# Performance work log

Measured on AMD Instinct MI355X. Metric: run time of the kernel, lower is better.

Reference implementation:

```python
import jax, jax.numpy as jnp
import numpy as np

N_EMBD = 768
N_HEAD = 12
HEAD_DIM = N_EMBD // N_HEAD
EPS = 1e-6


def setup_inputs() -> dict:
    key = jax.random.key(0)
    ks = jax.random.split(key, 8)
    B, T, C = 4, 2048, N_EMBD
    s = 0.02
    return {
        "x": jax.random.normal(ks[0], (B, T, C), jnp.float32),
        "ln1_w": jnp.ones((C,), jnp.float32),
        "ln1_b": jnp.zeros((C,), jnp.float32),
        "W_attn": jax.random.normal(ks[1], (C, 3 * C), jnp.float32) * s,
        "b_attn": jnp.zeros((3 * C,), jnp.float32),
        "W_attn_proj": jax.random.normal(ks[2], (C, C), jnp.float32) * s,
        "b_attn_proj": jnp.zeros((C,), jnp.float32),
        "ln2_w": jnp.ones((C,), jnp.float32),
        "ln2_b": jnp.zeros((C,), jnp.float32),
        "W_fc": jax.random.normal(ks[3], (C, 4 * C), jnp.float32) * s,
        "b_fc": jnp.zeros((4 * C,), jnp.float32),
        "W_mlp_proj": jax.random.normal(ks[4], (4 * C, C), jnp.float32) * s,
        "b_mlp_proj": jnp.zeros((C,), jnp.float32),
    }


def layer_norm(x, w, b):
    # Faithful to MyLayerNorm: (x - mean) / (std + eps), std with ddof=0
    mean = jnp.mean(x, axis=-1, keepdims=True)
    std = jnp.sqrt(jnp.mean((x - mean) ** 2, axis=-1, keepdims=True))
    return w * (x - mean) / (std + EPS) + b


def attention(h, W_attn, b_attn, W_proj, b_proj):
    B, T, C = h.shape
    qkv = h @ W_attn + b_attn                      # [B,T,3C]
    q, k, v = jnp.split(qkv, 3, axis=-1)
    # [B,T,C] -> [B,H,T,D]
    def to_heads(t):
        return t.reshape(B, T, N_HEAD, HEAD_DIM).transpose(0, 2, 1, 3)
    q, k, v = to_heads(q), to_heads(k), to_heads(v)
    att = jnp.einsum("bhtd,bhsd->bhts", q, k) * (1.0 / np.sqrt(HEAD_DIM))
    causal = jnp.tril(jnp.ones((T, T), bool))[None, None]
    att = jnp.where(causal, att, -jnp.inf)
    att = jax.nn.softmax(att, axis=-1)
    y = jnp.einsum("bhts,bhsd->bhtd", att, v)      # [B,H,T,D]
    y = y.transpose(0, 2, 1, 3).reshape(B, T, C)
    return y @ W_proj + b_proj


def mlp(h, W_fc, b_fc, W_proj, b_proj):
    h = jax.nn.gelu(h @ W_fc + b_fc, approximate=False)
    return h @ W_proj + b_proj


def reference(x, ln1_w, ln1_b, W_attn, b_attn, W_attn_proj, b_attn_proj,
              ln2_w, ln2_b, W_fc, b_fc, W_mlp_proj, b_mlp_proj):
    x = x + attention(layer_norm(x, ln1_w, ln1_b), W_attn, b_attn, W_attn_proj, b_attn_proj)
    x = x + mlp(layer_norm(x, ln2_w, ln2_b), W_fc, b_fc, W_mlp_proj, b_mlp_proj)
    return x
```

## Files before the change

### kernel.cpp

```cpp
#include <hip/hip_runtime.h>
#include <hip/hip_bf16.h>
#include <math.h>

#define N_EMBD 768
#define N_HEAD 12
#define HEAD_DIM 64
#define TOKENS 8192
#define SEQ 2048
#define BATCH 4
#define NQT (SEQ / 64)

typedef __attribute__((ext_vector_type(8))) short short8;
typedef __attribute__((ext_vector_type(4))) short short4v;
typedef __attribute__((ext_vector_type(4))) float f32x4;

__device__ __forceinline__ short f2bf(float f) {
    unsigned u = __builtin_bit_cast(unsigned, f);
    unsigned r = (u + 0x7fffu + ((u >> 16) & 1u)) >> 16;
    return (short)r;
}
__device__ __forceinline__ short f2bf_fast(float f) {
    unsigned u = __builtin_bit_cast(unsigned, f);
    return (short)((u + 0x8000u) >> 16);
}

__device__ __forceinline__ float gelu_fast(float x) {
    float z = 1.5957691216057308f * x * (1.0f + 0.044715f * x * x);
    return x / (1.0f + __expf(-z));
}

__device__ __forceinline__ void gld16(const void* g, void* l) {
    __builtin_amdgcn_global_load_lds(
        (const __attribute__((address_space(1))) unsigned int*)g,
        (__attribute__((address_space(3))) unsigned int*)l, 16, 0, 0);
}

__global__ __launch_bounds__(256) void wT_all(
        const float* __restrict__ Wa, short* __restrict__ Ta,
        const float* __restrict__ Wp, short* __restrict__ Tp,
        const float* __restrict__ Wf, short* __restrict__ Tf,
        const float* __restrict__ Wm, short* __restrict__ Tm) {
    __shared__ float T[32][33];
    int id = blockIdx.x;
    const float* W; short* Wt; int K, N;
    if (id < 1728)      { W = Wa; Wt = Ta; K = 768;  N = 2304; }
    else if (id < 2304) { W = Wp; Wt = Tp; K = 768;  N = 768;  id -= 1728; }
    else if (id < 4608) { W = Wf; Wt = Tf; K = 768;  N = 3072; id -= 2304; }
    else                { W = Wm; Wt = Tm; K = 3072; N = 768;  id -= 4608; }
    int tn = N >> 5;
    int n0 = (id % tn) * 32, k0 = (id / tn) * 32;
    int c = threadIdx.x & 31, r0 = threadIdx.x >> 5;
#pragma unroll
    for (int i = 0; i < 32; i += 8)
        T[r0 + i][c] = W[(size_t)(k0 + r0 + i) * N + n0 + c];
    __syncthreads();
#pragma unroll
    for (int i = 0; i < 32; i += 8)
        Wt[(size_t)(n0 + r0 + i) * K + k0 + c] = f2bf(T[c][r0 + i]);
}

__global__ __launch_bounds__(256) void ln_bf_kernel(const float* __restrict__ x,
                                                    const float* __restrict__ w,
                                                    const float* __restrict__ b,
                                                    short* __restrict__ out) {
    int row = blockIdx.x * 4 + (threadIdx.x >> 6);
    int lane = threadIdx.x & 63;
    const float4* xr = (const float4*)(x + (size_t)row * N_EMBD);
    const float4* wr = (const float4*)w;
    const float4* br = (const float4*)b;

    float4 v[3];
#pragma unroll
    for (int i = 0; i < 3; ++i) v[i] = xr[lane + 64 * i];
    float s = 0.f;
#pragma unroll
    for (int i = 0; i < 3; ++i) s += v[i].x + v[i].y + v[i].z + v[i].w;
#pragma unroll
    for (int off = 1; off < 64; off <<= 1) s += __shfl_xor(s, off, 64);
    float mean = s * (1.f / 768.f);

    float var = 0.f;
#pragma unroll
    for (int i = 0; i < 3; ++i) {
        float a0 = v[i].x - mean, a1 = v[i].y - mean,
              a2 = v[i].z - mean, a3 = v[i].w - mean;
        var += a0 * a0 + a1 * a1 + a2 * a2 + a3 * a3;
    }
#pragma unroll
    for (int off = 1; off < 64; off <<= 1) var += __shfl_xor(var, off, 64);
    float inv = 1.f / (sqrtf(var * (1.f / 768.f)) + 1e-6f);

    short4v* yr = (short4v*)(out + (size_t)row * N_EMBD);
#pragma unroll
    for (int i = 0; i < 3; ++i) {
        float4 wv = wr[lane + 64 * i], bv = br[lane + 64 * i];
        short4v o;
        o[0] = f2bf(wv.x * (v[i].x - mean) * inv + bv.x);
        o[1] = f2bf(wv.y * (v[i].y - mean) * inv + bv.y);
        o[2] = f2bf(wv.z * (v[i].z - mean) * inv + bv.z);
        o[3] = f2bf(wv.w * (v[i].w - mean) * inv + bv.w);
        yr[lane + 64 * i] = o;
    }
}

template <int ACT, int VOUT, int SWAP>
__global__ __launch_bounds__(256) void gemm_mfma(
        const short* __restrict__ A,
        const short* __restrict__ Bt,
        const float* __restrict__ bias,
        short* __restrict__ outp,
        short* __restrict__ vt,
        int M, int N, int K) {
    __shared__ short As[8192];
    __shared__ short Bs[8192];
    int tid = threadIdx.x;
    int wave = tid >> 6, lane = tid & 63;
    int quad = lane >> 4, l15 = lane & 15;
    int m0 = blockIdx.x * 128, n0 = blockIdx.y * 128;
    int wm = wave >> 1, wn = wave & 1;
    int sr = lane >> 2, sc = (lane & 3) * 8;

    f32x4 acc[4][4];
#pragma unroll
    for (int i = 0; i < 4; ++i)
#pragma unroll
        for (int j = 0; j < 4; ++j) acc[i][j] = (f32x4){0.f, 0.f, 0.f, 0.f};

    const short* ag = A + (size_t)(m0 + wave * 32 + sr) * K + sc;
    const short* bg = Bt + (size_t)(n0 + wave * 32 + sr) * K + sc;
    int woff = wave * 1024;
    int nk = K >> 5;

    auto stage = [&](int t) {
        int nb = (t & 1) * 4096 + woff;
        int kn = t << 5;
        gld16(ag + kn, &As[nb]);
        gld16(ag + kn + (size_t)16 * K, &As[nb + 512]);
        gld16(bg + kn, &Bs[nb]);
        gld16(bg + kn + (size_t)16 * K, &Bs[nb + 512]);
    };

    stage(0);
    if (nk > 1) stage(1);

    for (int it = 0; it < nk; ++it) {
        if (it + 1 < nk) asm volatile("s_waitcnt vmcnt(4)" ::: "memory");
        else             asm volatile("s_waitcnt vmcnt(0)" ::: "memory");
        __builtin_amdgcn_s_barrier();
        __builtin_amdgcn_sched_barrier(0);
        int cb = (it & 1) * 4096;
        short8 af[4], bfr[4];
#pragma unroll
        for (int mt = 0; mt < 4; ++mt)
            af[mt] = *(const short8*)&As[cb + (wm * 64 + mt * 16 + l15) * 32 + quad * 8];
#pragma unroll
        for (int nt = 0; nt < 4; ++nt)
            bfr[nt] = *(const short8*)&Bs[cb + (wn * 64 + nt * 16 + l15) * 32 + quad * 8];
        asm volatile("s_waitcnt lgkmcnt(0)" ::: "memory");
        __builtin_amdgcn_sched_barrier(0);
        __builtin_amdgcn_s_setprio(1);
#pragma unroll
        for (int mt = 0; mt < 4; ++mt)
#pragma unroll
            for (int nt = 0; nt < 4; ++nt) {
                if (SWAP)
                    acc[mt][nt] = __builtin_amdgcn_mfma_f32_16x16x32_bf16(
                        bfr[nt], af[mt], acc[mt][nt], 0, 0, 0);
                else
                    acc[mt][nt] = __builtin_amdgcn_mfma_f32_16x16x32_bf16(
                        af[mt], bfr[nt], acc[mt][nt], 0, 0, 0);
            }
        __builtin_amdgcn_s_setprio(0);
        __builtin_amdgcn_sched_barrier(0);
        __builtin_amdgcn_s_barrier();
        if (it + 2 < nk) stage(it + 2);
    }

    if (SWAP) {
#pragma unroll
        for (int nt = 0; nt < 4; ++nt) {
            int colb = n0 + wn * 64 + nt * 16 + quad * 4;
            f32x4 b4 = *(const f32x4*)&bias[colb];
#pragma unroll
            for (int mt = 0; mt < 4; ++mt) {
                int row = m0 + wm * 64 + mt * 16 + l15;
                short4v o4;
#pragma unroll
                for (int r = 0; r < 4; ++r) {
                    float v = acc[mt][nt][r] + b4[r];
                    if (ACT) v = gelu_fast(v);
                    o4[r] = f2bf(v);
                }
                *(short4v*)&outp[(size_t)row * N + colb] = o4;
            }
        }
        return;
    }

    if (VOUT && n0 >= 1536) {
#pragma unroll
        for (int mt = 0; mt < 4; ++mt) {
            int row0 = m0 + wm * 64 + mt * 16 + quad * 4;
            int b = row0 >> 11, t0 = row0 & 2047;
#pragma unroll
            for (int nt = 0; nt < 4; ++nt) {
                int col = n0 + wn * 64 + nt * 16 + l15;
                int vcol = col - 1536;
                int bh = b * N_HEAD + (vcol >> 6);
                int d = vcol & 63;
                float bi = bias[col];
                short4v o;
#pragma unroll
                for (int r = 0; r < 4; ++r) o[r] = f2bf(acc[mt][nt][r] + bi);
                *(short4v*)&vt[((size_t)bh * 64 + d) * SEQ + t0] = o;
            }
        }
        return;
    }

#pragma unroll
    for (int mt = 0; mt < 4; ++mt) {
        int row0 = m0 + wm * 64 + mt * 16 + quad * 4;
#pragma unroll
        for (int nt = 0; nt < 4; ++nt) {
            int col = n0 + wn * 64 + nt * 16 + l15;
            float bi = bias[col];
#pragma unroll
            for (int r = 0; r < 4; ++r) {
                float v = acc[mt][nt][r] + bi;
                if (ACT) v = gelu_fast(v);
                outp[(size_t)(row0 + r) * N + col] = f2bf(v);
            }
        }
    }
}

__global__ __launch_bounds__(256) void gemm_mfma_n64(
        const short* __restrict__ A,
        const short* __restrict__ Bt,
        const float* __restrict__ bias,
        const float* __restrict__ res,
        float* __restrict__ outp,
        int M, int N, int K) {
    __shared__ short As[8192];
    __shared__ short Bs[4096];
    int tid = threadIdx.x;
    int wave = tid >> 6, lane = tid & 63;
    int quad = lane >> 4, l15 = lane & 15;
    int m0 = blockIdx.x * 128, n0 = blockIdx.y * 64;
    int wm = wave >> 1, wn = wave & 1;
    int sr = lane >> 2, sc = (lane & 3) * 8;

    f32x4 acc[4][2];
#pragma unroll
    for (int i = 0; i < 4; ++i)
#pragma unroll
        for (int j = 0; j < 2; ++j) acc[i][j] = (f32x4){0.f, 0.f, 0.f, 0.f};

    const short* gptr[3];
    int loff[3];
    bool isa[3];
#pragma unroll
    for (int j = 0; j < 3; ++j) {
        int c = wave * 3 + j;
        if (c < 8) {
            gptr[j] = A + (size_t)(m0 + c * 16 + sr) * K + sc;
            loff[j] = c * 512; isa[j] = true;
        } else {
            gptr[j] = Bt + (size_t)(n0 + (c - 8) * 16 + sr) * K + sc;
            loff[j] = (c - 8) * 512; isa[j] = false;
        }
    }
    int nk = K >> 5;

    auto stage = [&](int t) {
        int nba = (t & 1) * 4096, nbb = (t & 1) * 2048;
        int kn = t << 5;
#pragma unroll
        for (int j = 0; j < 3; ++j)
            gld16(gptr[j] + kn, isa[j] ? &As[nba + loff[j]] : &Bs[nbb + loff[j]]);
    };

    stage(0);
    if (nk > 1) stage(1);

    for (int it = 0; it < nk; ++it) {
        if (it + 1 < nk) asm volatile("s_waitcnt vmcnt(3)" ::: "memory");
        else             asm volatile("s_waitcnt vmcnt(0)" ::: "memory");
        __builtin_amdgcn_s_barrier();
        __builtin_amdgcn_sched_barrier(0);
        int cba = (it & 1) * 4096, cbb = (it & 1) * 2048;
        short8 af[4], bfr[2];
#pragma unroll
        for (int mt = 0; mt < 4; ++mt)
            af[mt] = *(const short8*)&As[cba + (wm * 64 + mt * 16 + l15) * 32 + quad * 8];
#pragma unroll
        for (int nt = 0; nt < 2; ++nt)
            bfr[nt] = *(const short8*)&Bs[cbb + (wn * 32 + nt * 16 + l15) * 32 + quad * 8];
        asm volatile("s_waitcnt lgkmcnt(0)" ::: "memory");
        __builtin_amdgcn_sched_barrier(0);
        __builtin_amdgcn_s_setprio(1);
#pragma unroll
        for (int mt = 0; mt < 4; ++mt)
#pragma unroll
            for (int nt = 0; nt < 2; ++nt)
                acc[mt][nt] = __builtin_amdgcn_mfma_f32_16x16x32_bf16(
                    bfr[nt], af[mt], acc[mt][nt], 0, 0, 0);
        __builtin_amdgcn_s_setprio(0);
        __builtin_amdgcn_sched_barrier(0);
        __builtin_amdgcn_s_barrier();
        if (it + 2 < nk) stage(it + 2);
    }

#pragma unroll
    for (int nt = 0; nt < 2; ++nt) {
        int colb = n0 + wn * 32 + nt * 16 + quad * 4;
        f32x4 b4 = *(const f32x4*)&bias[colb];
#pragma unroll
        for (int mt = 0; mt < 4; ++mt) {
            int row = m0 + wm * 64 + mt * 16 + l15;
            f32x4 rv = *(const f32x4*)&res[(size_t)row * N + colb];
            f32x4 ov;
#pragma unroll
            for (int r = 0; r < 4; ++r) ov[r] = acc[mt][nt][r] + b4[r] + rv[r];
            *(f32x4*)&outp[(size_t)row * N + colb] = ov;
        }
    }
}

template <bool DIAG>
__device__ __forceinline__ void attn_kt(
        const short* __restrict__ Ks, const short* __restrict__ Vs,
        short* __restrict__ Ps, int cb,
        const short8* qf, short8 ones,
        f32x4* o, f32x4& lacc,
        int wave, int quad, int l15, int pswz) {
    f32x4 sacc[4];
#pragma unroll
    for (int nt = 0; nt < 4; ++nt) sacc[nt] = (f32x4){0.f, 0.f, 0.f, 0.f};
#pragma unroll
    for (int nt = 0; nt < 4; ++nt)
#pragma unroll
        for (int ks = 0; ks < 2; ++ks) {
            short8 kf = *(const short8*)&Ks[cb + ks * 2048 + (nt * 16 + l15) * 32 + quad * 8];
            sacc[nt] = __builtin_amdgcn_mfma_f32_16x16x32_bf16(qf[ks], kf, sacc[nt], 0, 0, 0);
        }

#pragma unroll
    for (int nt = 0; nt < 4; ++nt) {
        int scol = nt * 16 + l15;
        int base = (scol >> 5) * 2048 + (scol & 31);
#pragma unroll
        for (int r = 0; r < 4; ++r) {
            float p = exp2f(fmaf(sacc[nt][r], 0.18033688011112042f,
                                 -5.770780163555854f));
            if (DIAG && (scol > wave * 16 + quad * 4 + r)) p = 0.f;
            Ps[(base + (wave * 16 + quad * 4 + r) * 32) ^ (quad << 4)] = f2bf_fast(p);
        }
    }

    short8 pf0 = *(const short8*)&Ps[((wave * 16 + l15) * 32 + quad * 8) ^ pswz];
    short8 pf1 = *(const short8*)&Ps[(2048 + (wave * 16 + l15) * 32 + quad * 8) ^ pswz];
    lacc = __builtin_amdgcn_mfma_f32_16x16x32_bf16(pf0, ones, lacc, 0, 0, 0);
    lacc = __builtin_amdgcn_mfma_f32_16x16x32_bf16(pf1, ones, lacc, 0, 0, 0);
#pragma unroll
    for (int nt = 0; nt < 4; ++nt) {
        short8 vf0 = *(const short8*)&Vs[cb + (nt * 16 + l15) * 32 + quad * 8];
        short8 vf1 = *(const short8*)&Vs[cb + 2048 + (nt * 16 + l15) * 32 + quad * 8];
        o[nt] = __builtin_amdgcn_mfma_f32_16x16x32_bf16(pf0, vf0, o[nt], 0, 0, 0);
        o[nt] = __builtin_amdgcn_mfma_f32_16x16x32_bf16(pf1, vf1, o[nt], 0, 0, 0);
    }
}

__device__ __forceinline__ void attn_tile(
        const short* __restrict__ qkv, const short* __restrict__ Vt,
        short* __restrict__ y, int bh, int qt,
        short* Ks, short* Vs, short* Ps) {
    int tid = threadIdx.x;
    int wave = tid >> 6, lane = tid & 63;
    int quad = lane >> 4, l15 = lane & 15;
    int h = bh % N_HEAD, b = bh / N_HEAD;
    size_t bT = (size_t)b * SEQ;
    int q0 = qt * 64;
    int sr = lane >> 2, sc = (lane & 3) * 8;

    const short ONE_BF = (short)0x3F80;
    short8 ones;
#pragma unroll
    for (int j = 0; j < 8; ++j) ones[j] = ONE_BF;

    const short* qrow = qkv + (bT + q0 + wave * 16 + l15) * 2304 + h * 64 + quad * 8;
    short8 qf[2];
    qf[0] = *(const short8*)qrow;
    qf[1] = *(const short8*)(qrow + 32);

    __syncthreads();
#pragma unroll
    for (int j = 0; j < 4; ++j) {
        int c = wave * 4 + j;
        if (c < 8) {
            int sub = c >> 2, r0 = (c & 3) * 16;
            const short* g = qkv + (bT + r0 + sr) * 2304 + 768 + h * 64 + sub * 32 + sc;
            gld16(g, &Ks[sub * 2048 + r0 * 32]);
        } else {
            int cv = c - 8;
            int sub = cv >> 2, r0 = (cv & 3) * 16;
            const short* g = Vt + ((size_t)bh * 64 + r0 + sr) * SEQ + sub * 32 + sc;
            gld16(g, &Vs[sub * 2048 + r0 * 32]);
        }
    }
    __syncthreads();

    f32x4 o[4];
#pragma unroll
    for (int nt = 0; nt < 4; ++nt) o[nt] = (f32x4){0.f, 0.f, 0.f, 0.f};
    f32x4 lacc = (f32x4){0.f, 0.f, 0.f, 0.f};

    const int pswz = ((l15 >> 2) & 3) << 4;

    for (int kt = 0; kt < qt; ++kt) {
        int cb = (kt & 1) * 4096;
        if (kt) __syncthreads();
        int nb = ((kt + 1) & 1) * 4096;
        int k0n = (kt + 1) * 64;
#pragma unroll
        for (int j = 0; j < 4; ++j) {
            int c = wave * 4 + j;
            if (c < 8) {
                int sub = c >> 2, r0 = (c & 3) * 16;
                const short* g = qkv + (bT + k0n + r0 + sr) * 2304 + 768 + h * 64 + sub * 32 + sc;
                gld16(g, &Ks[nb + sub * 2048 + r0 * 32]);
            } else {
                int cv = c - 8;
                int sub = cv >> 2, r0 = (cv & 3) * 16;
                const short* g = Vt + ((size_t)bh * 64 + r0 + sr) * SEQ + k0n + sub * 32 + sc;
                gld16(g, &Vs[nb + sub * 2048 + r0 * 32]);
            }
        }
        attn_kt<false>(Ks, Vs, Ps, cb, qf, ones, o, lacc, wave, quad, l15, pswz);
    }

    if (qt) __syncthreads();
    attn_kt<true>(Ks, Vs, Ps, (qt & 1) * 4096, qf, ones, o, lacc,
                  wave, quad, l15, pswz);

    float inv[4];
#pragma unroll
    for (int r = 0; r < 4; ++r) inv[r] = 1.f / lacc[r];
#pragma unroll
    for (int nt = 0; nt < 4; ++nt)
#pragma unroll
        for (int r = 0; r < 4; ++r)
            y[(bT + q0 + wave * 16 + quad * 4 + r) * N_EMBD + h * 64 + nt * 16 + l15] =
                f2bf(o[nt][r] * inv[r]);
}

__global__ __launch_bounds__(256, 4) void attn_mfma(
        const short* __restrict__ qkv, const short* __restrict__ Vt,
        short* __restrict__ y) {
    __shared__ short Ks[8192], Vs[8192], Ps[4096];
    int bh = blockIdx.x;
    int pair = blockIdx.y;
    attn_tile(qkv, Vt, y, bh, pair, Ks, Vs, Ps);
    attn_tile(qkv, Vt, y, bh, NQT - 1 - pair, Ks, Vs, Ps);
}

extern "C" void kernel_launch(void* const* d_in, const int* in_sizes, int n_in,
                              void* d_out, int out_size, void* d_ws, size_t ws_size,
                              hipStream_t stream) {
    const float* x         = (const float*)d_in[0];
    const float* ln1_w     = (const float*)d_in[1];
    const float* ln1_b     = (const float*)d_in[2];
    const float* W_attn    = (const float*)d_in[3];
    const float* b_attn    = (const float*)d_in[4];
    const float* W_attn_pr = (const float*)d_in[5];
    const float* b_attn_pr = (const float*)d_in[6];
    const float* ln2_w     = (const float*)d_in[7];
    const float* ln2_b     = (const float*)d_in[8];
    const float* W_fc      = (const float*)d_in[9];
    const float* b_fc      = (const float*)d_in[10];
    const float* W_mlp_pr  = (const float*)d_in[11];
    const float* b_mlp_pr  = (const float*)d_in[12];
    float* out = (float*)d_out;

    const int M = TOKENS, C = N_EMBD;
    char* ws = (char*)d_ws;
    size_t region0 = (size_t)M * 3072 * 2;
    short* qkv_bf = (short*)ws;
    short* fc_bf  = (short*)ws;
    size_t off = region0;
    short* VtB   = (short*)(ws + off); off += (size_t)48 * 64 * SEQ * 2;
    short* yb    = (short*)(ws + off); off += (size_t)M * C * 2;
    short* lnb   = (short*)(ws + off); off += (size_t)M * C * 2;
    float* x1    = (float*)(ws + off); off += (size_t)M * C * 4;
    short* WaT   = (short*)(ws + off); off += (size_t)2304 * 768 * 2;
    short* WpT   = (short*)(ws + off); off += (size_t)768 * 768 * 2;
    short* WfT   = (short*)(ws + off); off += (size_t)3072 * 768 * 2;
    short* WmT   = (short*)(ws + off); off += (size_t)768 * 3072 * 2;

    wT_all<<<6912, 256, 0, stream>>>(W_attn, WaT, W_attn_pr, WpT,
                                     W_fc, WfT, W_mlp_pr, WmT);

    ln_bf_kernel<<<M / 4, 256, 0, stream>>>(x, ln1_w, ln1_b, lnb);

    gemm_mfma<0, 1, 0><<<dim3(M / 128, 2304 / 128), 256, 0, stream>>>(
        lnb, WaT, b_attn, qkv_bf, VtB, M, 2304, 768);

    attn_mfma<<<dim3(BATCH * N_HEAD, NQT / 2), 256, 0, stream>>>(qkv_bf, VtB, yb);

    gemm_mfma_n64<<<dim3(M / 128, 768 / 64), 256, 0, stream>>>(
        yb, WpT, b_attn_pr, x, x1, M, 768, 768);

    ln_bf_kernel<<<M / 4, 256, 0, stream>>>(x1, ln2_w, ln2_b, lnb);

    gemm_mfma<1, 0, 1><<<dim3(M / 128, 3072 / 128), 256, 0, stream>>>(
        lnb, WfT, b_fc, fc_bf, nullptr, M, 3072, 768);

    gemm_mfma_n64<<<dim3(M / 128, 768 / 64), 256, 0, stream>>>(
        fc_bf, WmT, b_mlp_pr, x1, out, M, 768, 3072);
}
```

Baseline: 389.7 us.

## Switch GEMM main loops to single-barrier double buffering and deepen n64 K-step

```diff
diff --git a/kernel.cpp b/kernel.cpp
--- a/kernel.cpp
+++ b/kernel.cpp
@@ -129,26 +129,24 @@
     const short* ag = A + (size_t)(m0 + wave * 32 + sr) * K + sc;
     const short* bg = Bt + (size_t)(n0 + wave * 32 + sr) * K + sc;
     int woff = wave * 1024;
+
+    gld16(ag, &As[woff]);
+    gld16(ag + (size_t)16 * K, &As[woff + 512]);
+    gld16(bg, &Bs[woff]);
+    gld16(bg + (size_t)16 * K, &Bs[woff + 512]);
+
     int nk = K >> 5;
-
-    auto stage = [&](int t) {
-        int nb = (t & 1) * 4096 + woff;
-        int kn = t << 5;
-        gld16(ag + kn, &As[nb]);
-        gld16(ag + kn + (size_t)16 * K, &As[nb + 512]);
-        gld16(bg + kn, &Bs[nb]);
-        gld16(bg + kn + (size_t)16 * K, &Bs[nb + 512]);
-    };
-
-    stage(0);
-    if (nk > 1) stage(1);
-
     for (int it = 0; it < nk; ++it) {
-        if (it + 1 < nk) asm volatile("s_waitcnt vmcnt(4)" ::: "memory");
-        else             asm volatile("s_waitcnt vmcnt(0)" ::: "memory");
-        __builtin_amdgcn_s_barrier();
-        __builtin_amdgcn_sched_barrier(0);
         int cb = (it & 1) * 4096;
+        __syncthreads();
+        if (it + 1 < nk) {
+            int nb = ((it + 1) & 1) * 4096 + woff;
+            int kn = (it + 1) << 5;
+            gld16(ag + kn, &As[nb]);
+            gld16(ag + kn + (size_t)16 * K, &As[nb + 512]);
+            gld16(bg + kn, &Bs[nb]);
+            gld16(bg + kn + (size_t)16 * K, &Bs[nb + 512]);
+        }
         short8 af[4], bfr[4];
 #pragma unroll
         for (int mt = 0; mt < 4; ++mt)
@@ -156,9 +154,6 @@
 #pragma unroll
         for (int nt = 0; nt < 4; ++nt)
             bfr[nt] = *(const short8*)&Bs[cb + (wn * 64 + nt * 16 + l15) * 32 + quad * 8];
-        asm volatile("s_waitcnt lgkmcnt(0)" ::: "memory");
-        __builtin_amdgcn_sched_barrier(0);
-        __builtin_amdgcn_s_setprio(1);
 #pragma unroll
         for (int mt = 0; mt < 4; ++mt)
 #pragma unroll
@@ -170,10 +165,6 @@
                     acc[mt][nt] = __builtin_amdgcn_mfma_f32_16x16x32_bf16(
                         af[mt], bfr[nt], acc[mt][nt], 0, 0, 0);
             }
-        __builtin_amdgcn_s_setprio(0);
-        __builtin_amdgcn_sched_barrier(0);
-        __builtin_amdgcn_s_barrier();
-        if (it + 2 < nk) stage(it + 2);
     }
 
     if (SWAP) {
@@ -242,8 +233,8 @@
         const float* __restrict__ res,
         float* __restrict__ outp,
         int M, int N, int K) {
-    __shared__ short As[8192];
-    __shared__ short Bs[4096];
+    __shared__ short As[16384];
+    __shared__ short Bs[8192];
     int tid = threadIdx.x;
     int wave = tid >> 6, lane = tid & 63;
     int quad = lane >> 4, l15 = lane & 15;
@@ -257,59 +248,57 @@
 #pragma unroll
         for (int j = 0; j < 2; ++j) acc[i][j] = (f32x4){0.f, 0.f, 0.f, 0.f};
 
-    const short* gptr[3];
-    int loff[3];
-    bool isa[3];
-#pragma unroll
-    for (int j = 0; j < 3; ++j) {
-        int c = wave * 3 + j;
-        if (c < 8) {
-            gptr[j] = A + (size_t)(m0 + c * 16 + sr) * K + sc;
-            loff[j] = c * 512; isa[j] = true;
+    const short* gptr[6];
+    int loff[6];
+    bool isa[6];
+#pragma unroll
+    for (int j = 0; j < 6; ++j) {
+        int c = wave * 6 + j;
+        if (c < 16) {
+            int ks = c >> 3, r0 = (c & 7) * 16;
+            gptr[j] = A + (size_t)(m0 + r0 + sr) * K + ks * 32 + sc;
+            loff[j] = ks * 4096 + r0 * 32; isa[j] = true;
         } else {
-            gptr[j] = Bt + (size_t)(n0 + (c - 8) * 16 + sr) * K + sc;
-            loff[j] = (c - 8) * 512; isa[j] = false;
-        }
-    }
-    int nk = K >> 5;
+            int cb = c - 16;
+            int ks = cb >> 2, r0 = (cb & 3) * 16;
+            gptr[j] = Bt + (size_t)(n0 + r0 + sr) * K + ks * 32 + sc;
+            loff[j] = ks * 2048 + r0 * 32; isa[j] = false;
+        }
+    }
+    int nk = K >> 6;
 
     auto stage = [&](int t) {
-        int nba = (t & 1) * 4096, nbb = (t & 1) * 2048;
-        int kn = t << 5;
-#pragma unroll
-        for (int j = 0; j < 3; ++j)
-            gld16(gptr[j] + kn, isa[j] ? &As[nba + loff[j]] : &Bs[nbb + loff[j]]);
+        int ba = (t & 1) << 13, bb = (t & 1) << 12;
+        int kn = t << 6;
+#pragma unroll
+        for (int j = 0; j < 6; ++j)
+            gld16(gptr[j] + kn, isa[j] ? &As[ba + loff[j]] : &Bs[bb + loff[j]]);
     };
 
     stage(0);
-    if (nk > 1) stage(1);
 
     for (int it = 0; it < nk; ++it) {
-        if (it + 1 < nk) asm volatile("s_waitcnt vmcnt(3)" ::: "memory");
-        else             asm volatile("s_waitcnt vmcnt(0)" ::: "memory");
-        __builtin_amdgcn_s_barrier();
-        __builtin_amdgcn_sched_barrier(0);
-        int cba = (it & 1) * 4096, cbb = (it & 1) * 2048;
-        short8 af[4], bfr[2];
-#pragma unroll
-        for (int mt = 0; mt < 4; ++mt)
-            af[mt] = *(const short8*)&As[cba + (wm * 64 + mt * 16 + l15) * 32 + quad * 8];
-#pragma unroll
-        for (int nt = 0; nt < 2; ++nt)
-            bfr[nt] = *(const short8*)&Bs[cbb + (wn * 32 + nt * 16 + l15) * 32 + quad * 8];
-        asm volatile("s_waitcnt lgkmcnt(0)" ::: "memory");
-        __builtin_amdgcn_sched_barrier(0);
-        __builtin_amdgcn_s_setprio(1);
-#pragma unroll
-        for (int mt = 0; mt < 4; ++mt)
+        int cba = (it & 1) << 13, cbb = (it & 1) << 12;
+        __syncthreads();
+        if (it + 1 < nk) stage(it + 1);
+#pragma unroll
+        for (int ks = 0; ks < 2; ++ks) {
+            short8 af[4], bfr[2];
+#pragma unroll
+            for (int mt = 0; mt < 4; ++mt)
+                af[mt] = *(const short8*)&As[cba + ks * 4096 +
+                                             (wm * 64 + mt * 16 + l15) * 32 + quad * 8];
 #pragma unroll
             for (int nt = 0; nt < 2; ++nt)
-                acc[mt][nt] = __builtin_amdgcn_mfma_f32_16x16x32_bf16(
-                    bfr[nt], af[mt], acc[mt][nt], 0, 0, 0);
-        __builtin_amdgcn_s_setprio(0);
-        __builtin_amdgcn_sched_barrier(0);
-        __builtin_amdgcn_s_barrier();
-        if (it + 2 < nk) stage(it + 2);
+                bfr[nt] = *(const short8*)&Bs[cbb + ks * 2048 +
+                                              (wn * 32 + nt * 16 + l15) * 32 + quad * 8];
+#pragma unroll
+            for (int mt = 0; mt < 4; ++mt)
+#pragma unroll
+                for (int nt = 0; nt < 2; ++nt)
+                    acc[mt][nt] = __builtin_amdgcn_mfma_f32_16x16x32_bf16(
+                        bfr[nt], af[mt], acc[mt][nt], 0, 0, 0);
+        }
     }
 
 #pragma unroll
```

Result: faster. 376.9 us (-3.3%).
